# Kernel optimization log

Hardware: AMD Instinct MI355X
Metric: run time of the kernel (lower is better)

Reference implementation:

```python
import jax, jax.numpy as jnp
import numpy as np

SEQ, D_IN, D_OUT = 4096, 768, 768

def setup_inputs() -> dict:
    key = jax.random.key(0)
    kx, kq, kk, kv = jax.random.split(key, 4)
    s = 1.0 / np.sqrt(D_IN)
    return {
        "x": jax.random.normal(kx, (SEQ, D_IN), dtype=jnp.float32),
        "Wq": jax.random.uniform(kq, (D_IN, D_OUT), jnp.float32, -s, s),
        "Wk": jax.random.uniform(kk, (D_IN, D_OUT), jnp.float32, -s, s),
        "Wv": jax.random.uniform(kv, (D_IN, D_OUT), jnp.float32, -s, s),
    }

def reference(x, Wq, Wk, Wv):
    # x: [S, d_in]; Wq/Wk/Wv: [d_in, d_out] (torch nn.Linear weight transposed)
    q = x @ Wq
    k = x @ Wk
    v = x @ Wv
    scores = (q @ k.T) / jnp.sqrt(jnp.asarray(k.shape[1], q.dtype))  # [S, S]
    weights = jax.nn.softmax(scores, axis=1)
    return weights @ v  # [S, d_out]
```

## Files before the change

### kernel.cpp

```cpp
#include <hip/hip_runtime.h>
#include <hip/hip_bf16.h>

typedef __bf16 bf16x8 __attribute__((ext_vector_type(8)));
typedef float  f32x4  __attribute__((ext_vector_type(4)));
typedef float  f4     __attribute__((ext_vector_type(4)));
typedef unsigned short us4 __attribute__((ext_vector_type(4)));
typedef unsigned short us8 __attribute__((ext_vector_type(8)));

__device__ inline unsigned short f2bf(float f) {
  union { float f; unsigned int u; } v; v.f = f;
  unsigned int r = v.u + 0x7fffu + ((v.u >> 16) & 1u);
  return (unsigned short)(r >> 16);
}
__device__ inline float bf2f(unsigned short u) {
  union { unsigned int u; float f; } v; v.u = (unsigned int)u << 16;
  return v.f;
}

__device__ inline void gload_lds16(const void* g, void* l) {
  __builtin_amdgcn_global_load_lds((const __attribute__((address_space(1))) void*)g,
                                   (__attribute__((address_space(3))) void*)l, 16, 0, 0);
}

__global__ __launch_bounds__(256) void convx(const float* __restrict__ x,
                                             unsigned short* __restrict__ xb) {
  int i = blockIdx.x * 256 + threadIdx.x;
  f4 v = ((const f4*)x)[i];
  us4 o;
  #pragma unroll
  for (int c = 0; c < 4; ++c) o[c] = f2bf(v[c]);
  ((us4*)xb)[i] = o;
}

__global__ __launch_bounds__(256) void convw(const float* __restrict__ Wq,
                                             const float* __restrict__ Wk,
                                             const float* __restrict__ Wv,
                                             unsigned short* __restrict__ wt) {
  __shared__ unsigned short tile[32][33];
  const float* W = blockIdx.z == 0 ? Wq : (blockIdx.z == 1 ? Wk : Wv);
  int k0 = blockIdx.x * 32, n0 = blockIdx.y * 32;
  int c = threadIdx.x & 31, r8 = threadIdx.x >> 5;
  #pragma unroll
  for (int p = 0; p < 4; ++p) {
    int r = p * 8 + r8;
    tile[r][c] = f2bf(W[(size_t)(k0 + r) * 768 + n0 + c]);
  }
  __syncthreads();
  #pragma unroll
  for (int p = 0; p < 4; ++p) {
    int r = p * 8 + r8;
    wt[((size_t)blockIdx.z * 768 + n0 + r) * 768 + k0 + c] = tile[c][r];
  }
}

__global__ __launch_bounds__(256) void transv(const unsigned short* __restrict__ qkv,
                                              unsigned short* __restrict__ vt) {
  __shared__ unsigned short tile[32][33];
  int s0 = blockIdx.x * 32, d0 = blockIdx.y * 32;
  int c = threadIdx.x & 31, r8 = threadIdx.x >> 5;
  #pragma unroll
  for (int p = 0; p < 4; ++p) {
    int r = p * 8 + r8;
    tile[r][c] = qkv[(size_t)(s0 + r) * 2304 + 1536 + d0 + c];
  }
  __syncthreads();
  #pragma unroll
  for (int p = 0; p < 4; ++p) {
    int r = p * 8 + r8;
    vt[(size_t)(d0 + r) * 4096 + s0 + c] = tile[c][r];
  }
}

template <int WAVES, int WM, int WN, typename OUT_T, bool DOEXP, bool DOSCALE>
__global__ __launch_bounds__(WAVES * 64, 2) void gemmdp(const unsigned short* __restrict__ A,
                                                        const unsigned short* __restrict__ B,
                                                        OUT_T* __restrict__ C0,
                                                        OUT_T* __restrict__ C1,
                                                        const float* __restrict__ rowinv,
                                                        int lda, int ldb, int ldc, int kspan,
                                                        int nbx, float cscale) {
  constexpr int BM = WAVES * 32, BN = WAVES * 32;
  constexpr int MF = 2 * WAVES / WM, NF = 2 * WAVES / WN;
  constexpr int SLOT = (BM + BN) * 64;
  __shared__ __align__(16) char lds[4 * SLOT];
  const int tid = threadIdx.x;
  const int w = tid >> 6, l = tid & 63;
  const int wr = w / WN, wc = w % WN;
  const int lr = l & 15, lk = l >> 4;

  const int nwg = gridDim.x;
  const int swz = (blockIdx.x & 7) * (nwg >> 3) + (blockIdx.x >> 3);
  const int bx = swz % nbx, by = swz / nbx;
  const int m0 = by * BM, n0 = bx * BN;
  const int koff0 = blockIdx.y * kspan;
  OUT_T* __restrict__ C = blockIdx.y ? C1 : C0;

  f32x4 acc[MF][NF] = {};

  const int trow = tid >> 2;
  const int koff = ((tid & 3) * 8) ^ (((tid >> 5) & 1) * 16);
  const unsigned short* gA0 = A + (size_t)(m0 + trow) * lda + koff + koff0;
  const unsigned short* gA1 = A + (size_t)(m0 + BM / 2 + trow) * lda + koff + koff0;
  const unsigned short* gB0 = B + (size_t)(n0 + trow) * ldb + koff + koff0;
  const unsigned short* gB1 = B + (size_t)(n0 + BN / 2 + trow) * ldb + koff + koff0;
  const int wave16 = (tid & ~63) * 16;

  auto stage = [&](int slot, int k0) {
    char* base = lds + slot * SLOT;
    gload_lds16(gA0 + k0, base + wave16);
    gload_lds16(gA1 + k0, base + BM * 32 + wave16);
    gload_lds16(gB0 + k0, base + BM * 64 + wave16);
    gload_lds16(gB1 + k0, base + BM * 64 + BN * 32 + wave16);
  };

  const int xorv = ((l >> 3) & 1) << 5;
  const int aoff = (wr * (MF * 16) + lr) * 64 + lk * 16;
  const int boff = BM * 64 + (wc * (NF * 16) + lr) * 64 + lk * 16;

  const int nsteps = kspan >> 5;
  stage(0, 0); stage(1, 32); stage(2, 64);

  for (int s = 0; s < nsteps; ++s) {
    __builtin_amdgcn_sched_barrier(0);
    if (s < nsteps - 2)       asm volatile("s_waitcnt vmcnt(8)" ::: "memory");
    else if (s == nsteps - 2) asm volatile("s_waitcnt vmcnt(4)" ::: "memory");
    else                      asm volatile("s_waitcnt vmcnt(0)" ::: "memory");
    __builtin_amdgcn_s_barrier();
    __builtin_amdgcn_sched_barrier(0);

    if (s + 3 < nsteps) stage((s + 3) & 3, (s + 3) << 5);

    const char* sb = lds + (s & 3) * SLOT;
    bf16x8 fa[MF], fb[NF];
    #pragma unroll
    for (int mf = 0; mf < MF; ++mf)
      fa[mf] = *(const bf16x8*)(sb + ((aoff + mf * 1024) ^ xorv));
    #pragma unroll
    for (int nf = 0; nf < NF; ++nf)
      fb[nf] = *(const bf16x8*)(sb + ((boff + nf * 1024) ^ xorv));

    __builtin_amdgcn_s_setprio(1);
    #pragma unroll
    for (int mf = 0; mf < MF; ++mf)
      #pragma unroll
      for (int nf = 0; nf < NF; ++nf)
        acc[mf][nf] = __builtin_amdgcn_mfma_f32_16x16x32_bf16(fa[mf], fb[nf], acc[mf][nf], 0, 0, 0);
    __builtin_amdgcn_s_setprio(0);
  }

  #pragma unroll
  for (int mf = 0; mf < MF; ++mf)
    #pragma unroll
    for (int nf = 0; nf < NF; ++nf)
      #pragma unroll
      for (int i = 0; i < 4; ++i) {
        int r = m0 + wr * (MF * 16) + mf * 16 + lk * 4 + i;
        int c = n0 + wc * (NF * 16) + nf * 16 + lr;
        float v = acc[mf][nf][i] * cscale;
        if constexpr (DOEXP)   v = __expf(v);
        if constexpr (DOSCALE) v *= rowinv[r];
        if constexpr (__is_same(OUT_T, unsigned short)) C[(size_t)r * ldc + c] = f2bf(v);
        else                                            C[(size_t)r * ldc + c] = v;
      }
}

__global__ __launch_bounds__(256) void rowsum(const unsigned short* __restrict__ P,
                                              float* __restrict__ rowinv) {
  const int wv = threadIdx.x >> 6, l = threadIdx.x & 63;
  const int r = blockIdx.x * 4 + wv;
  const unsigned short* row = P + (size_t)r * 4096;
  float sum = 0.f;
  #pragma unroll
  for (int j = 0; j < 8; ++j) {
    us8 v = ((const us8*)row)[l + j * 64];
    #pragma unroll
    for (int c = 0; c < 8; ++c) sum += bf2f(v[c]);
  }
  #pragma unroll
  for (int o = 32; o > 0; o >>= 1) sum += __shfl_xor(sum, o);
  if (l == 0) rowinv[r] = 1.f / sum;
}

__global__ __launch_bounds__(256) void reduce_add(float* __restrict__ out,
                                                  const float* __restrict__ p1) {
  int i = blockIdx.x * 256 + threadIdx.x;
  f4 a = ((const f4*)out)[i];
  f4 b = ((const f4*)p1)[i];
  #pragma unroll
  for (int c = 0; c < 4; ++c) a[c] += b[c];
  ((f4*)out)[i] = a;
}

extern "C" void kernel_launch(void* const* d_in, const int* in_sizes, int n_in,
                              void* d_out, int out_size, void* d_ws, size_t ws_size,
                              hipStream_t stream) {
  const float* x  = (const float*)d_in[0];
  const float* Wq = (const float*)d_in[1];
  const float* Wk = (const float*)d_in[2];
  const float* Wv = (const float*)d_in[3];
  float* out = (float*)d_out;
  char* ws = (char*)d_ws;

  unsigned short* qkv = (unsigned short*)ws;
  unsigned short* P   = (unsigned short*)(ws + 18874368);
  unsigned short* xb  = (unsigned short*)(ws + 18874368);
  unsigned short* wt  = (unsigned short*)(ws + 18874368 + 6291456);
  unsigned short* vt  = (unsigned short*)(ws + 52428800);
  float* rowinvp      = (float*)(ws + 58720256);
  float* pvpart       = (float*)ws;

  const float qscale = 0.03608439182435161f;

  convx<<<3072, 256, 0, stream>>>(x, xb);
  convw<<<dim3(24, 24, 3), 256, 0, stream>>>(Wq, Wk, Wv, wt);
  gemmdp<4, 2, 2, unsigned short, false, false><<<576, 256, 0, stream>>>(
      xb, wt, qkv, qkv, nullptr, 768, 768, 2304, 768, 18, 1.0f);
  transv<<<dim3(128, 24), 256, 0, stream>>>(qkv, vt);
  gemmdp<8, 2, 4, unsigned short, true, false><<<256, 512, 0, stream>>>(
      qkv, qkv + 768, P, P, nullptr, 2304, 2304, 4096, 768, 16, qscale);
  rowsum<<<1024, 256, 0, stream>>>(P, rowinvp);
  gemmdp<4, 2, 2, float, false, true><<<dim3(192, 2), 256, 0, stream>>>(
      P, vt, out, pvpart, rowinvp, 4096, 4096, 768, 2048, 6, 1.0f);
  reduce_add<<<3072, 256, 0, stream>>>(out, pvpart);
}
```

Measured before the change: 119.5 us.

## Fuse conversion kernels, use 3-slot LDS ring, split PV GEMM K four ways

Merges the x and weight bf16 conversion kernels into one launch. Makes the GEMM LDS ring depth a template parameter, using 3 slots with a minimum of 3 workgroups per CU for the 128x128 GEMMs, which aims to raise occupancy. Raises the PV GEMM split-K from 2 to 4, giving 768 workgroups instead of 384 to better fill the CUs. In exchange, a 4-way reduce kernel must read and write more partial buffers in extra workspace, and the shallower prefetch ring hides less memory latency.

```diff
diff --git a/kernel.cpp b/kernel.cpp
--- a/kernel.cpp
+++ b/kernel.cpp
@@ -22,34 +22,38 @@
                                    (__attribute__((address_space(3))) void*)l, 16, 0, 0);
 }
 
-__global__ __launch_bounds__(256) void convx(const float* __restrict__ x,
-                                             unsigned short* __restrict__ xb) {
-  int i = blockIdx.x * 256 + threadIdx.x;
-  f4 v = ((const f4*)x)[i];
-  us4 o;
-  #pragma unroll
-  for (int c = 0; c < 4; ++c) o[c] = f2bf(v[c]);
-  ((us4*)xb)[i] = o;
-}
-
-__global__ __launch_bounds__(256) void convw(const float* __restrict__ Wq,
-                                             const float* __restrict__ Wk,
-                                             const float* __restrict__ Wv,
-                                             unsigned short* __restrict__ wt) {
+__global__ __launch_bounds__(256) void convfused(const float* __restrict__ x,
+                                                 const float* __restrict__ Wq,
+                                                 const float* __restrict__ Wk,
+                                                 const float* __restrict__ Wv,
+                                                 unsigned short* __restrict__ xb,
+                                                 unsigned short* __restrict__ wt) {
   __shared__ unsigned short tile[32][33];
-  const float* W = blockIdx.z == 0 ? Wq : (blockIdx.z == 1 ? Wk : Wv);
-  int k0 = blockIdx.x * 32, n0 = blockIdx.y * 32;
-  int c = threadIdx.x & 31, r8 = threadIdx.x >> 5;
-  #pragma unroll
-  for (int p = 0; p < 4; ++p) {
-    int r = p * 8 + r8;
-    tile[r][c] = f2bf(W[(size_t)(k0 + r) * 768 + n0 + c]);
-  }
-  __syncthreads();
-  #pragma unroll
-  for (int p = 0; p < 4; ++p) {
-    int r = p * 8 + r8;
-    wt[((size_t)blockIdx.z * 768 + n0 + r) * 768 + k0 + c] = tile[c][r];
+  if (blockIdx.x < 3072) {
+    int i = blockIdx.x * 256 + threadIdx.x;
+    f4 v = ((const f4*)x)[i];
+    us4 o;
+    #pragma unroll
+    for (int c = 0; c < 4; ++c) o[c] = f2bf(v[c]);
+    ((us4*)xb)[i] = o;
+  } else {
+    int b = blockIdx.x - 3072;
+    int bz = b / 576, rem = b % 576;
+    int bx = rem / 24, by = rem % 24;
+    const float* W = bz == 0 ? Wq : (bz == 1 ? Wk : Wv);
+    int k0 = bx * 32, n0 = by * 32;
+    int c = threadIdx.x & 31, r8 = threadIdx.x >> 5;
+    #pragma unroll
+    for (int p = 0; p < 4; ++p) {
+      int r = p * 8 + r8;
+      tile[r][c] = f2bf(W[(size_t)(k0 + r) * 768 + n0 + c]);
+    }
+    __syncthreads();
+    #pragma unroll
+    for (int p = 0; p < 4; ++p) {
+      int r = p * 8 + r8;
+      wt[((size_t)bz * 768 + n0 + r) * 768 + k0 + c] = tile[c][r];
+    }
   }
 }
 
@@ -71,18 +75,20 @@
   }
 }
 
-template <int WAVES, int WM, int WN, typename OUT_T, bool DOEXP, bool DOSCALE>
-__global__ __launch_bounds__(WAVES * 64, 2) void gemmdp(const unsigned short* __restrict__ A,
-                                                        const unsigned short* __restrict__ B,
-                                                        OUT_T* __restrict__ C0,
-                                                        OUT_T* __restrict__ C1,
-                                                        const float* __restrict__ rowinv,
-                                                        int lda, int ldb, int ldc, int kspan,
-                                                        int nbx, float cscale) {
+template <int WAVES, int WM, int WN, int RING, int MINW, typename OUT_T, bool DOEXP, bool DOSCALE>
+__global__ __launch_bounds__(WAVES * 64, MINW) void gemmdp(const unsigned short* __restrict__ A,
+                                                           const unsigned short* __restrict__ B,
+                                                           OUT_T* __restrict__ C0,
+                                                           OUT_T* __restrict__ C1,
+                                                           OUT_T* __restrict__ C2,
+                                                           OUT_T* __restrict__ C3,
+                                                           const float* __restrict__ rowinv,
+                                                           int lda, int ldb, int ldc, int kspan,
+                                                           int nbx, float cscale) {
   constexpr int BM = WAVES * 32, BN = WAVES * 32;
   constexpr int MF = 2 * WAVES / WM, NF = 2 * WAVES / WN;
   constexpr int SLOT = (BM + BN) * 64;
-  __shared__ __align__(16) char lds[4 * SLOT];
+  __shared__ __align__(16) char lds[RING * SLOT];
   const int tid = threadIdx.x;
   const int w = tid >> 6, l = tid & 63;
   const int wr = w / WN, wc = w % WN;
@@ -93,7 +99,7 @@
   const int bx = swz % nbx, by = swz / nbx;
   const int m0 = by * BM, n0 = bx * BN;
   const int koff0 = blockIdx.y * kspan;
-  OUT_T* __restrict__ C = blockIdx.y ? C1 : C0;
+  OUT_T* __restrict__ C = blockIdx.y == 0 ? C0 : (blockIdx.y == 1 ? C1 : (blockIdx.y == 2 ? C2 : C3));
 
   f32x4 acc[MF][NF] = {};
 
@@ -118,19 +124,26 @@
   const int boff = BM * 64 + (wc * (NF * 16) + lr) * 64 + lk * 16;
 
   const int nsteps = kspan >> 5;
-  stage(0, 0); stage(1, 32); stage(2, 64);
-
+  #pragma unroll
+  for (int j = 0; j < RING - 1; ++j) stage(j, j * 32);
+
+  int rdslot = 0, stslot = RING - 1;
   for (int s = 0; s < nsteps; ++s) {
     __builtin_amdgcn_sched_barrier(0);
-    if (s < nsteps - 2)       asm volatile("s_waitcnt vmcnt(8)" ::: "memory");
-    else if (s == nsteps - 2) asm volatile("s_waitcnt vmcnt(4)" ::: "memory");
-    else                      asm volatile("s_waitcnt vmcnt(0)" ::: "memory");
+    if constexpr (RING == 4) {
+      if (s < nsteps - 2)       asm volatile("s_waitcnt vmcnt(8)" ::: "memory");
+      else if (s == nsteps - 2) asm volatile("s_waitcnt vmcnt(4)" ::: "memory");
+      else                      asm volatile("s_waitcnt vmcnt(0)" ::: "memory");
+    } else {
+      if (s < nsteps - 1)       asm volatile("s_waitcnt vmcnt(4)" ::: "memory");
+      else                      asm volatile("s_waitcnt vmcnt(0)" ::: "memory");
+    }
     __builtin_amdgcn_s_barrier();
     __builtin_amdgcn_sched_barrier(0);
 
-    if (s + 3 < nsteps) stage((s + 3) & 3, (s + 3) << 5);
-
-    const char* sb = lds + (s & 3) * SLOT;
+    if (s + RING - 1 < nsteps) stage(stslot, (s + RING - 1) << 5);
+
+    const char* sb = lds + rdslot * SLOT;
     bf16x8 fa[MF], fb[NF];
     #pragma unroll
     for (int mf = 0; mf < MF; ++mf)
@@ -146,6 +159,9 @@
       for (int nf = 0; nf < NF; ++nf)
         acc[mf][nf] = __builtin_amdgcn_mfma_f32_16x16x32_bf16(fa[mf], fb[nf], acc[mf][nf], 0, 0, 0);
     __builtin_amdgcn_s_setprio(0);
+
+    rdslot = (rdslot + 1 == RING) ? 0 : rdslot + 1;
+    stslot = (stslot + 1 == RING) ? 0 : stslot + 1;
   }
 
   #pragma unroll
@@ -181,13 +197,17 @@
   if (l == 0) rowinv[r] = 1.f / sum;
 }
 
-__global__ __launch_bounds__(256) void reduce_add(float* __restrict__ out,
-                                                  const float* __restrict__ p1) {
+__global__ __launch_bounds__(256) void reduce_add4(float* __restrict__ out,
+                                                   const float* __restrict__ p1,
+                                                   const float* __restrict__ p2,
+                                                   const float* __restrict__ p3) {
   int i = blockIdx.x * 256 + threadIdx.x;
   f4 a = ((const f4*)out)[i];
   f4 b = ((const f4*)p1)[i];
-  #pragma unroll
-  for (int c = 0; c < 4; ++c) a[c] += b[c];
+  f4 c = ((const f4*)p2)[i];
+  f4 d = ((const f4*)p3)[i];
+  #pragma unroll
+  for (int k = 0; k < 4; ++k) a[k] += b[k] + c[k] + d[k];
   ((f4*)out)[i] = a;
 }
 
@@ -207,19 +227,20 @@
   unsigned short* wt  = (unsigned short*)(ws + 18874368 + 6291456);
   unsigned short* vt  = (unsigned short*)(ws + 52428800);
   float* rowinvp      = (float*)(ws + 58720256);
-  float* pvpart       = (float*)ws;
+  float* p1           = (float*)ws;
+  float* p2           = (float*)(ws + 58736640);
+  float* p3           = (float*)(ws + 58736640 + 12582912);
 
   const float qscale = 0.03608439182435161f;
 
-  convx<<<3072, 256, 0, stream>>>(x, xb);
-  convw<<<dim3(24, 24, 3), 256, 0, stream>>>(Wq, Wk, Wv, wt);
-  gemmdp<4, 2, 2, unsigned short, false, false><<<576, 256, 0, stream>>>(
-      xb, wt, qkv, qkv, nullptr, 768, 768, 2304, 768, 18, 1.0f);
+  convfused<<<4800, 256, 0, stream>>>(x, Wq, Wk, Wv, xb, wt);
+  gemmdp<4, 2, 2, 3, 3, unsigned short, false, false><<<576, 256, 0, stream>>>(
+      xb, wt, qkv, qkv, qkv, qkv, nullptr, 768, 768, 2304, 768, 18, 1.0f);
   transv<<<dim3(128, 24), 256, 0, stream>>>(qkv, vt);
-  gemmdp<8, 2, 4, unsigned short, true, false><<<256, 512, 0, stream>>>(
-      qkv, qkv + 768, P, P, nullptr, 2304, 2304, 4096, 768, 16, qscale);
+  gemmdp<8, 2, 4, 4, 2, unsigned short, true, false><<<256, 512, 0, stream>>>(
+      qkv, qkv + 768, P, P, P, P, nullptr, 2304, 2304, 4096, 768, 16, qscale);
   rowsum<<<1024, 256, 0, stream>>>(P, rowinvp);
-  gemmdp<4, 2, 2, float, false, true><<<dim3(192, 2), 256, 0, stream>>>(
-      P, vt, out, pvpart, rowinvp, 4096, 4096, 768, 2048, 6, 1.0f);
-  reduce_add<<<3072, 256, 0, stream>>>(out, pvpart);
-}
+  gemmdp<4, 2, 2, 3, 3, float, false, true><<<dim3(192, 4), 256, 0, stream>>>(
+      P, vt, out, p1, p2, p3, rowinvp, 4096, 4096, 768, 1024, 6, 1.0f);
+  reduce_add4<<<3072, 256, 0, stream>>>(out, p1, p2, p3);
+}
```

Measured after the change: 119.7 us. About the same (+0.2%).
